# Kernel tuning notes

Hardware: AMD Instinct MI355X
Metric: run time of the kernel (lower is better)

Reference implementation:

```python
import jax, jax.numpy as jnp
import numpy as np

B, S, D, H = 4, 2048, 1024, 16
DH = D // H
SCALE = float(np.sqrt(DH))


def setup_inputs() -> dict:
    key = jax.random.key(0)
    ks = jax.random.split(key, 5)
    std = 1.0 / np.sqrt(D)
    return {
        "x": jax.random.normal(ks[0], (B, S, D), dtype=jnp.float32),
        "Wq": jax.random.normal(ks[1], (D, D), dtype=jnp.float32) * std,
        "bq": jnp.zeros((D,), dtype=jnp.float32),
        "Wk": jax.random.normal(ks[2], (D, D), dtype=jnp.float32) * std,
        "bk": jnp.zeros((D,), dtype=jnp.float32),
        "Wv": jax.random.normal(ks[3], (D, D), dtype=jnp.float32) * std,
        "bv": jnp.zeros((D,), dtype=jnp.float32),
        "Wo": jax.random.normal(ks[4], (D, D), dtype=jnp.float32) * std,
        "bo": jnp.zeros((D,), dtype=jnp.float32),
        "padding_mask": jnp.ones((B, S), dtype=jnp.int32),
    }


def reference(x, Wq, bq, Wk, bk, Wv, bv, Wo, bo, padding_mask):
    b, s, d = x.shape
    # QKV projections, split heads -> [b, h, s, dh]
    q = (x @ Wq + bq).reshape(b, s, H, DH).transpose(0, 2, 1, 3)
    k = (x @ Wk + bk).reshape(b, s, H, DH).transpose(0, 2, 1, 3)
    v = (x @ Wv + bv).reshape(b, s, H, DH).transpose(0, 2, 1, 3)
    # scaled scores [b, h, s, s]
    scores = jnp.einsum('bhqd,bhkd->bhqk', q, k) / SCALE
    neg_inf = jnp.float32(-jnp.inf)
    causal = jnp.tril(jnp.ones((s, s), dtype=bool))  # [s, s]
    scores = jnp.where(causal[None, None, :, :], scores, neg_inf)
    pad = (padding_mask != 0)[:, None, None, :]  # [b,1,1,s] on key axis
    scores = jnp.where(pad, scores, neg_inf)
    weights = jax.nn.softmax(scores, axis=-1)
    weights = jnp.nan_to_num(weights, nan=0.0)  # fully-masked rows -> 0
    # dropout is identity in eval / p=0
    attended = jnp.einsum('bhqk,bhkd->bhqd', weights, v)
    attended = attended.transpose(0, 2, 1, 3).reshape(b, s, d)
    return attended @ Wo + bo
```

## Files before the change

kernel.cpp:

```cpp
#include <hip/hip_runtime.h>
#include <hip/hip_bf16.h>

#define B_   4
#define S_   2048
#define D_   1024
#define H_   16
#define DH_  64
#define M_   (B_ * S_)

typedef __attribute__((ext_vector_type(8))) short  bfrag8;
typedef __attribute__((ext_vector_type(4))) float  facc4;
typedef unsigned short u16;
typedef unsigned long long u64;

__device__ __forceinline__ u16 f2bf(float f) {
    union { __hip_bfloat16 h; u16 u; } c;
    c.h = __float2bfloat16(f);
    return c.u;
}

__device__ __forceinline__ u16 bfr(float f) {
    unsigned b = __float_as_uint(f);
    return (u16)((b + 0x7FFFu + ((b >> 16) & 1u)) >> 16);
}

__device__ __forceinline__ void gl_lds16(const u16* g, u16* l) {
    __builtin_amdgcn_global_load_lds((const __attribute__((address_space(1))) void*)g,
                                     (__attribute__((address_space(3))) void*)l,
                                     16, 0, 0);
}

__global__ __launch_bounds__(256) void prep(const float* __restrict__ x, u16* __restrict__ X16,
                                            const float* __restrict__ w0, const float* __restrict__ w1,
                                            const float* __restrict__ w2, const float* __restrict__ w3,
                                            u16* __restrict__ o0, u16* __restrict__ o1,
                                            u16* __restrict__ o2, u16* __restrict__ o3) {
    __shared__ u16 t[32][33];
    int bid = blockIdx.x;
    if (bid < 4096) {
        int i = (bid * 256 + threadIdx.x) * 8;
        float4 v0 = *(const float4*)(x + i);
        float4 v1 = *(const float4*)(x + i + 4);
        ushort4 r0, r1;
        r0.x = f2bf(v0.x); r0.y = f2bf(v0.y); r0.z = f2bf(v0.z); r0.w = f2bf(v0.w);
        r1.x = f2bf(v1.x); r1.y = f2bf(v1.y); r1.z = f2bf(v1.z); r1.w = f2bf(v1.w);
        *(ushort4*)(X16 + i) = r0;
        *(ushort4*)(X16 + i + 4) = r1;
    } else {
        int lid = bid - 4096;
        int z = lid >> 10, r = lid & 1023;
        const float* w; u16* o;
        switch (z) {
            case 0: w = w0; o = o0; break;
            case 1: w = w1; o = o1; break;
            case 2: w = w2; o = o2; break;
            default: w = w3; o = o3; break;
        }
        int kb = (r >> 5) * 32, nb = (r & 31) * 32;
        int c = threadIdx.x & 31, r0 = threadIdx.x >> 5;
#pragma unroll
        for (int i = 0; i < 4; i++) {
            int rr = r0 + 8 * i;
            t[rr][c] = f2bf(w[(kb + rr) * D_ + nb + c]);
        }
        __syncthreads();
#pragma unroll
        for (int i = 0; i < 4; i++) {
            int rr = r0 + 8 * i;
            o[(nb + rr) * D_ + kb + c] = t[c][rr];
        }
    }
}

#define ABUF_ (256 * 32)
#define TBUF_ ((256 + 128) * 32)
#define NKT_  32

__device__ __forceinline__ void gemm_body256(const u16* __restrict__ A,
                                             const u16* __restrict__ BT,
                                             const float* __restrict__ bias,
                                             void* __restrict__ Cout, int mode, float scale,
                                             u16* S, int nb, int mb) {
    int tid = threadIdx.x;
    int w = tid >> 6, lane = tid & 63, quad = lane >> 4, l16 = lane & 15;
    int wm = (w >> 1) * 64, wn = (w & 1) * 64;
    int x3 = l16 & 3;

    const u16* Aga[2]; const u16* Bga;
#pragma unroll
    for (int i = 0; i < 2; ++i) {
        int idx = i * 512 + tid, row = idx >> 2;
        int lu = (idx & 3) ^ (row & 3);
        Aga[i] = A + (size_t)(mb + row) * D_ + lu * 8;
    }
    {
        int row = tid >> 2;
        int lu = (tid & 3) ^ (row & 3);
        Bga = BT + (size_t)(nb + row) * D_ + lu * 8;
    }

    facc4 acc[4][4] = {};

    u16* Bu0 = S;
    u16* Bu1 = S + TBUF_;
    u16* Bu2 = S + 2 * TBUF_;

    auto stage = [&](u16* Nb, int ko) {
#pragma unroll
        for (int i = 0; i < 2; ++i) gl_lds16(Aga[i] + ko, Nb + (i * 512 + tid) * 8);
        gl_lds16(Bga + ko, Nb + ABUF_ + tid * 8);
    };
    auto compute = [&](const u16* Cb) {
        int pu = (quad ^ x3) * 8;
        bfrag8 af[4], bf[4];
#pragma unroll
        for (int mt = 0; mt < 4; ++mt)
            af[mt] = *(const bfrag8*)(Cb + (wm + mt * 16 + l16) * 32 + pu);
#pragma unroll
        for (int nt = 0; nt < 4; ++nt)
            bf[nt] = *(const bfrag8*)(Cb + ABUF_ + (wn + nt * 16 + l16) * 32 + pu);
        __builtin_amdgcn_s_setprio(1);
#pragma unroll
        for (int mt = 0; mt < 4; ++mt)
#pragma unroll
            for (int nt = 0; nt < 4; ++nt)
                acc[mt][nt] = __builtin_amdgcn_mfma_f32_16x16x32_bf16(af[mt], bf[nt], acc[mt][nt], 0, 0, 0);
        __builtin_amdgcn_s_setprio(0);
    };

    stage(Bu0, 0);
    stage(Bu1, 32);

    u16 *bc = Bu0, *bn = Bu1, *bs = Bu2;
    for (int kt = 0; kt < NKT_; ++kt) {
        if (kt < NKT_ - 1) asm volatile("s_waitcnt vmcnt(3)" ::: "memory");
        else               asm volatile("s_waitcnt vmcnt(0)" ::: "memory");
        __builtin_amdgcn_sched_barrier(0);
        __builtin_amdgcn_s_barrier();
        __builtin_amdgcn_sched_barrier(0);
        if (kt + 2 < NKT_) stage(bs, (kt + 2) * 32);
        compute(bc);
        u16* tmp = bc; bc = bn; bn = bs; bs = tmp;
    }

#pragma unroll
    for (int mt = 0; mt < 4; ++mt) {
        int m_base = mb + wm + mt * 16 + quad * 4;
#pragma unroll
        for (int nt = 0; nt < 4; ++nt) {
            int n = nb + wn + nt * 16 + l16;
            float bv = bias[n];
            int h = n >> 6, dd = n & 63;
#pragma unroll
            for (int r = 0; r < 4; ++r) {
                int m = m_base + r;
                float v = (acc[mt][nt][r] + bv) * scale;
                int bi = m >> 11, s = m & (S_ - 1);
                if (mode == 0) {
                    ((u16*)Cout)[(((bi * H_ + h) * S_) + s) * DH_ + dd] = bfr(v);
                } else if (mode == 1) {
                    ((u16*)Cout)[(((bi * H_ + h) * DH_) + dd) * S_ + s] = bfr(v);
                } else {
                    ((float*)Cout)[(size_t)m * D_ + n] = v;
                }
            }
        }
    }
}

#define CE_Q 0.18033688011112042f

__global__ __launch_bounds__(512, 4) void gemm_qkv(const u16* __restrict__ A,
                                                const u16* __restrict__ WTq, const float* __restrict__ bq, u16* __restrict__ Qb,
                                                const u16* __restrict__ WTk, const float* __restrict__ bk, u16* __restrict__ Kb,
                                                const u16* __restrict__ WTv, const float* __restrict__ bv, u16* __restrict__ VTb) {
    __shared__ __attribute__((aligned(16))) u16 Sh[3 * TBUF_];
    int lid = blockIdx.x;
    int xcd = lid & 7, s = lid >> 3;
    int z = s >> 5, inner = s & 31;
    int mb = (xcd * 4 + (inner >> 3)) * 256;
    int nb = (inner & 7) * 128;
    switch (z) {
        case 0: gemm_body256(A, WTq, bq, Qb, 0, CE_Q, Sh, nb, mb); break;
        case 1: gemm_body256(A, WTk, bk, Kb, 0, 1.0f, Sh, nb, mb); break;
        default: gemm_body256(A, WTv, bv, VTb, 1, 1.0f, Sh, nb, mb); break;
    }
}

__global__ __launch_bounds__(512, 4) void gemm_o(const u16* __restrict__ A,
                                              const u16* __restrict__ WTo, const float* __restrict__ bo,
                                              float* __restrict__ out) {
    __shared__ __attribute__((aligned(16))) u16 Sh[3 * TBUF_];
    int lid = blockIdx.x;
    int xcd = lid & 7, s = lid >> 3;
    int mb = (xcd * 4 + (s >> 3)) * 256;
    int nb = (s & 7) * 128;
    gemm_body256(A, WTo, bo, out, 2, 1.0f, Sh, nb, mb);
}

__device__ __forceinline__ void soft_pv(const float* p, float& lp, facc4* oaccq,
                                        const bfrag8* vf, int a0, int a1, bool qlo) {
    float rs = 0.f;
    unsigned pk[4];
#pragma unroll
    for (int j = 0; j < 4; ++j) {
        float e0 = exp2f(p[2 * j]);
        float e1 = exp2f(p[2 * j + 1]);
        rs += e0; rs += e1;
        pk[j] = __builtin_amdgcn_perm(__float_as_uint(e1), __float_as_uint(e0), 0x07060302u);
    }
    lp += rs;
    union { unsigned d[4]; bfrag8 v; } pb;
    {
        unsigned lo, hi;
        lo = __builtin_amdgcn_ds_bpermute(a0, (int)pk[0]);
        hi = __builtin_amdgcn_ds_bpermute(a0, (int)pk[2]);
        pb.d[0] = qlo ? lo : hi;
        lo = __builtin_amdgcn_ds_bpermute(a0, (int)pk[1]);
        hi = __builtin_amdgcn_ds_bpermute(a0, (int)pk[3]);
        pb.d[1] = qlo ? lo : hi;
        lo = __builtin_amdgcn_ds_bpermute(a1, (int)pk[0]);
        hi = __builtin_amdgcn_ds_bpermute(a1, (int)pk[2]);
        pb.d[2] = qlo ? lo : hi;
        lo = __builtin_amdgcn_ds_bpermute(a1, (int)pk[1]);
        hi = __builtin_amdgcn_ds_bpermute(a1, (int)pk[3]);
        pb.d[3] = qlo ? lo : hi;
    }
    __builtin_amdgcn_s_setprio(1);
#pragma unroll
    for (int dt = 0; dt < 4; ++dt)
        oaccq[dt] = __builtin_amdgcn_mfma_f32_16x16x32_bf16(vf[dt], pb.v, oaccq[dt], 0, 0, 0);
    __builtin_amdgcn_s_setprio(0);
}

__global__ __launch_bounds__(256, 4) void attn(const u16* __restrict__ Q,
                                               const u16* __restrict__ K,
                                               const u16* __restrict__ VT,
                                               const int* __restrict__ pm,
                                               u16* __restrict__ Aout) {
    __shared__ __attribute__((aligned(16))) u16 Ks[2][32 * 64];
    __shared__ __attribute__((aligned(16))) u16 Vs[2][64 * 32];
    __shared__ unsigned pms[64];

    int tid = threadIdx.x, w = tid >> 6, lane = tid & 63;
    int quad = lane >> 4, l16 = lane & 15;

    int lid = blockIdx.x;
    int bh  = (lid & 7) * 8 + ((lid >> 3) & 7);
    int g   = lid >> 6;
    int gq = g >> 2, gr = g & 3;
    int ci = (gq == 0) ? 15 - gr : (gq == 1) ? gr : (gq == 2) ? 11 - gr : 4 + gr;
    int b = bh >> 4, h = bh & 15;

    int qbase = ci * 128;
    int qw = qbase + w * 32;
    int tmax = (qbase >> 5) + 3;

    const u16* Qp = Q + (size_t)(b * H_ + h) * S_ * DH_;
    const u16* Kp = K + (size_t)(b * H_ + h) * S_ * DH_;
    const u16* Vp = VT + (size_t)(b * H_ + h) * DH_ * S_;
    u16* Ao = Aout + (size_t)b * S_ * D_ + h * DH_;

#pragma unroll
    for (int i = 0; i < 8; ++i) {
        int j2 = w * 16 + i * 2;
        u64 m = __ballot(pm[b * S_ + j2 * 32 + lane] != 0);
        if (lane == 0) { pms[j2] = (unsigned)m; pms[j2 + 1] = (unsigned)(m >> 32); }
    }

    int krow = tid >> 3, ku = tid & 7;
    const u16* Kg = Kp + krow * DH_ + ((ku ^ (krow & 7)) * 8);
    int vrow = tid >> 2, vu = tid & 3;
    const u16* Vg = Vp + vrow * S_ + ((vu ^ (vrow & 3)) * 8);
    u16* Kl[2] = { &Ks[0][tid * 8], &Ks[1][tid * 8] };
    u16* Vl[2] = { &Vs[0][tid * 8], &Vs[1][tid * 8] };

    int k7 = l16 & 7, v3 = l16 & 3;

    int a0 = ((((2 * quad) & 3) * 16 + l16) << 2);
    int a1 = ((((2 * quad + 1) & 3) * 16 + l16) << 2);
    bool qlo = quad < 2;

    bfrag8 qf[2][2];
#pragma unroll
    for (int qt = 0; qt < 2; ++qt)
#pragma unroll
        for (int cc = 0; cc < 2; ++cc)
            qf[qt][cc] = *(const bfrag8*)(Qp + (qw + qt * 16 + l16) * DH_ + cc * 32 + quad * 8);

    facc4 oacc[2][4] = {};
    float lp[2] = {0.f, 0.f};

    gl_lds16(Kg, Kl[0]);
    gl_lds16(Vg, Vl[0]);
    __syncthreads();
    unsigned vmn = pms[0];

    for (int t = 0; t <= tmax; ++t) {
        int cur = t & 1, nxt = cur ^ 1;
        unsigned vm = vmn;
        if (t < tmax) {
            int k1 = (t + 1) * 32;
            gl_lds16(Kg + k1 * DH_, Kl[nxt]);
            gl_lds16(Vg + k1, Vl[nxt]);
            vmn = pms[t + 1];
        }
        int k0 = t * 32;
        const u16* Kc = Ks[cur];
        const u16* Vc = Vs[cur];

        bfrag8 kf00 = *(const bfrag8*)(Kc + (l16 * 8        + ((quad)     ^ k7)) * 8);
        bfrag8 kf01 = *(const bfrag8*)(Kc + (l16 * 8        + ((quad + 4) ^ k7)) * 8);
        bfrag8 kf10 = *(const bfrag8*)(Kc + ((l16 + 16) * 8 + ((quad)     ^ k7)) * 8);
        bfrag8 kf11 = *(const bfrag8*)(Kc + ((l16 + 16) * 8 + ((quad + 4) ^ k7)) * 8);
        bfrag8 vf[4];
#pragma unroll
        for (int dt = 0; dt < 4; ++dt)
            vf[dt] = *(const bfrag8*)(Vc + ((dt * 16 + l16) * 4 + (quad ^ v3)) * 8);

        facc4 st[2][2] = {};
        __builtin_amdgcn_s_setprio(1);
#pragma unroll
        for (int qt = 0; qt < 2; ++qt) {
            st[qt][0] = __builtin_amdgcn_mfma_f32_16x16x32_bf16(kf00, qf[qt][0], st[qt][0], 0, 0, 0);
            st[qt][0] = __builtin_amdgcn_mfma_f32_16x16x32_bf16(kf01, qf[qt][1], st[qt][0], 0, 0, 0);
            st[qt][1] = __builtin_amdgcn_mfma_f32_16x16x32_bf16(kf10, qf[qt][0], st[qt][1], 0, 0, 0);
            st[qt][1] = __builtin_amdgcn_mfma_f32_16x16x32_bf16(kf11, qf[qt][1], st[qt][1], 0, 0, 0);
        }
        __builtin_amdgcn_s_setprio(0);

        if (vm == 0xffffffffu && k0 + 31 < qw) {
#pragma unroll
            for (int qt = 0; qt < 2; ++qt) {
                float p[8];
#pragma unroll
                for (int kt = 0; kt < 2; ++kt)
#pragma unroll
                    for (int r = 0; r < 4; ++r) p[kt * 4 + r] = st[qt][kt][r];
                soft_pv(p, lp[qt], oacc[qt], vf, a0, a1, qlo);
            }
        } else {
#pragma unroll
            for (int qt = 0; qt < 2; ++qt) {
                int q0 = qw + qt * 16;
                float p[8];
#pragma unroll
                for (int kt = 0; kt < 2; ++kt)
#pragma unroll
                    for (int r = 0; r < 4; ++r) {
                        int kl = kt * 16 + quad * 4 + r;
                        bool ok = ((vm >> kl) & 1u) && (k0 + kl <= q0 + l16);
                        p[kt * 4 + r] = ok ? st[qt][kt][r] : -1e30f;
                    }
                soft_pv(p, lp[qt], oacc[qt], vf, a0, a1, qlo);
            }
        }
        __syncthreads();
    }

#pragma unroll
    for (int qt = 0; qt < 2; ++qt) {
        float l = lp[qt];
        l += __shfl_xor(l, 16);
        l += __shfl_xor(l, 32);
        float linv = (l > 0.f) ? 1.f / l : 0.f;
        size_t qoff = (size_t)(qw + qt * 16 + l16) * D_;
#pragma unroll
        for (int dt = 0; dt < 4; ++dt) {
            union { u16 hh[4]; u64 q; } pk4;
#pragma unroll
            for (int r = 0; r < 4; ++r) pk4.hh[r] = bfr(oacc[qt][dt][r] * linv);
            *(u64*)(Ao + qoff + dt * 16 + quad * 4) = pk4.q;
        }
    }
}

extern "C" void kernel_launch(void* const* d_in, const int* in_sizes, int n_in,
                              void* d_out, int out_size, void* d_ws, size_t ws_size,
                              hipStream_t stream) {
    const float* x  = (const float*)d_in[0];
    const float* Wq = (const float*)d_in[1];
    const float* bq = (const float*)d_in[2];
    const float* Wk = (const float*)d_in[3];
    const float* bk = (const float*)d_in[4];
    const float* Wv = (const float*)d_in[5];
    const float* bv = (const float*)d_in[6];
    const float* Wo = (const float*)d_in[7];
    const float* bo = (const float*)d_in[8];
    const int*   pm = (const int*)d_in[9];
    float* out = (float*)d_out;

    char* ws = (char*)d_ws;
    const size_t SZ_XD = (size_t)M_ * D_ * 2;
    const size_t SZ_W  = (size_t)D_ * D_ * 2;
    u16* X16 = (u16*)ws;
    u16* WTq = (u16*)(ws + SZ_XD);
    u16* WTk = (u16*)(ws + SZ_XD + SZ_W);
    u16* WTv = (u16*)(ws + SZ_XD + 2 * SZ_W);
    u16* WTo = (u16*)(ws + SZ_XD + 3 * SZ_W);
    u16* Qb  = (u16*)(ws + SZ_XD + 4 * SZ_W);
    u16* Kb  = (u16*)(ws + 2 * SZ_XD + 4 * SZ_W);
    u16* VTb = (u16*)(ws + 3 * SZ_XD + 4 * SZ_W);
    u16* Att = X16;

    prep<<<dim3(8192), 256, 0, stream>>>(x, X16, Wq, Wk, Wv, Wo, WTq, WTk, WTv, WTo);

    gemm_qkv<<<dim3(768), 512, 0, stream>>>(X16, WTq, bq, Qb, WTk, bk, Kb, WTv, bv, VTb);

    attn<<<dim3(1024), 256, 0, stream>>>(Qb, Kb, VTb, pm, Att);

    gemm_o<<<dim3(256), 512, 0, stream>>>(Att, WTo, bo, out);
}
```

Before: 254.7 us.

## Shrink GEMM tiles to 128x128 and stage two K/V tiles per attention iteration

The projection GEMMs move from 256x128 tiles with 512 threads to 128x128 tiles with 256 threads, doubling the grid so the output GEMM gets 512 blocks instead of 256 and fills the CUs better. The attention kernel now loads 64 keys per pipeline stage (two 32-key sub-tiles) and processes both before each barrier, halving the number of syncthreads and global-to-LDS round trips. The cost is less operand reuse per GEMM tile, more LDS per attention block, and a coarser causal loop bound that may process some extra masked keys.

```diff
diff --git a/kernel.cpp b/kernel.cpp
--- a/kernel.cpp
+++ b/kernel.cpp
@@ -72,11 +72,11 @@
     }
 }
 
-#define ABUF_ (256 * 32)
-#define TBUF_ ((256 + 128) * 32)
-#define NKT_  32
-
-__device__ __forceinline__ void gemm_body256(const u16* __restrict__ A,
+#define AB2_ (128 * 32)
+#define TB2_ (256 * 32)
+#define NKT_ 32
+
+__device__ __forceinline__ void gemm_body128(const u16* __restrict__ A,
                                              const u16* __restrict__ BT,
                                              const float* __restrict__ bias,
                                              void* __restrict__ Cout, int mode, float scale,
@@ -86,29 +86,26 @@
     int wm = (w >> 1) * 64, wn = (w & 1) * 64;
     int x3 = l16 & 3;
 
-    const u16* Aga[2]; const u16* Bga;
+    const u16* Aga[2]; const u16* Bga[2];
 #pragma unroll
     for (int i = 0; i < 2; ++i) {
-        int idx = i * 512 + tid, row = idx >> 2;
+        int idx = i * 256 + tid, row = idx >> 2;
         int lu = (idx & 3) ^ (row & 3);
         Aga[i] = A + (size_t)(mb + row) * D_ + lu * 8;
-    }
-    {
-        int row = tid >> 2;
-        int lu = (tid & 3) ^ (row & 3);
-        Bga = BT + (size_t)(nb + row) * D_ + lu * 8;
+        Bga[i] = BT + (size_t)(nb + row) * D_ + lu * 8;
     }
 
     facc4 acc[4][4] = {};
 
     u16* Bu0 = S;
-    u16* Bu1 = S + TBUF_;
-    u16* Bu2 = S + 2 * TBUF_;
+    u16* Bu1 = S + TB2_;
+    u16* Bu2 = S + 2 * TB2_;
 
     auto stage = [&](u16* Nb, int ko) {
 #pragma unroll
-        for (int i = 0; i < 2; ++i) gl_lds16(Aga[i] + ko, Nb + (i * 512 + tid) * 8);
-        gl_lds16(Bga + ko, Nb + ABUF_ + tid * 8);
+        for (int i = 0; i < 2; ++i) gl_lds16(Aga[i] + ko, Nb + (i * 256 + tid) * 8);
+#pragma unroll
+        for (int i = 0; i < 2; ++i) gl_lds16(Bga[i] + ko, Nb + AB2_ + (i * 256 + tid) * 8);
     };
     auto compute = [&](const u16* Cb) {
         int pu = (quad ^ x3) * 8;
@@ -118,7 +115,7 @@
             af[mt] = *(const bfrag8*)(Cb + (wm + mt * 16 + l16) * 32 + pu);
 #pragma unroll
         for (int nt = 0; nt < 4; ++nt)
-            bf[nt] = *(const bfrag8*)(Cb + ABUF_ + (wn + nt * 16 + l16) * 32 + pu);
+            bf[nt] = *(const bfrag8*)(Cb + AB2_ + (wn + nt * 16 + l16) * 32 + pu);
         __builtin_amdgcn_s_setprio(1);
 #pragma unroll
         for (int mt = 0; mt < 4; ++mt)
@@ -133,7 +130,7 @@
 
     u16 *bc = Bu0, *bn = Bu1, *bs = Bu2;
     for (int kt = 0; kt < NKT_; ++kt) {
-        if (kt < NKT_ - 1) asm volatile("s_waitcnt vmcnt(3)" ::: "memory");
+        if (kt < NKT_ - 1) asm volatile("s_waitcnt vmcnt(4)" ::: "memory");
         else               asm volatile("s_waitcnt vmcnt(0)" ::: "memory");
         __builtin_amdgcn_sched_barrier(0);
         __builtin_amdgcn_s_barrier();
@@ -170,32 +167,32 @@
 
 #define CE_Q 0.18033688011112042f
 
-__global__ __launch_bounds__(512, 4) void gemm_qkv(const u16* __restrict__ A,
+__global__ __launch_bounds__(256, 3) void gemm_qkv(const u16* __restrict__ A,
                                                 const u16* __restrict__ WTq, const float* __restrict__ bq, u16* __restrict__ Qb,
                                                 const u16* __restrict__ WTk, const float* __restrict__ bk, u16* __restrict__ Kb,
                                                 const u16* __restrict__ WTv, const float* __restrict__ bv, u16* __restrict__ VTb) {
-    __shared__ __attribute__((aligned(16))) u16 Sh[3 * TBUF_];
+    __shared__ __attribute__((aligned(16))) u16 Sh[3 * TB2_];
     int lid = blockIdx.x;
-    int xcd = lid & 7, s = lid >> 3;
-    int z = s >> 5, inner = s & 31;
-    int mb = (xcd * 4 + (inner >> 3)) * 256;
-    int nb = (inner & 7) * 128;
+    int xcd = lid & 7, rest = lid >> 3;
+    int z = rest >> 6, r2 = rest & 63;
+    int mb = (xcd * 8 + (r2 >> 3)) * 128;
+    int nb = (r2 & 7) * 128;
     switch (z) {
-        case 0: gemm_body256(A, WTq, bq, Qb, 0, CE_Q, Sh, nb, mb); break;
-        case 1: gemm_body256(A, WTk, bk, Kb, 0, 1.0f, Sh, nb, mb); break;
-        default: gemm_body256(A, WTv, bv, VTb, 1, 1.0f, Sh, nb, mb); break;
-    }
-}
-
-__global__ __launch_bounds__(512, 4) void gemm_o(const u16* __restrict__ A,
+        case 0: gemm_body128(A, WTq, bq, Qb, 0, CE_Q, Sh, nb, mb); break;
+        case 1: gemm_body128(A, WTk, bk, Kb, 0, 1.0f, Sh, nb, mb); break;
+        default: gemm_body128(A, WTv, bv, VTb, 1, 1.0f, Sh, nb, mb); break;
+    }
+}
+
+__global__ __launch_bounds__(256, 3) void gemm_o(const u16* __restrict__ A,
                                               const u16* __restrict__ WTo, const float* __restrict__ bo,
                                               float* __restrict__ out) {
-    __shared__ __attribute__((aligned(16))) u16 Sh[3 * TBUF_];
+    __shared__ __attribute__((aligned(16))) u16 Sh[3 * TB2_];
     int lid = blockIdx.x;
-    int xcd = lid & 7, s = lid >> 3;
-    int mb = (xcd * 4 + (s >> 3)) * 256;
-    int nb = (s & 7) * 128;
-    gemm_body256(A, WTo, bo, out, 2, 1.0f, Sh, nb, mb);
+    int xcd = lid & 7, r2 = lid >> 3;
+    int mb = (xcd * 8 + (r2 >> 3)) * 128;
+    int nb = (r2 & 7) * 128;
+    gemm_body128(A, WTo, bo, out, 2, 1.0f, Sh, nb, mb);
 }
 
 __device__ __forceinline__ void soft_pv(const float* p, float& lp, facc4* oaccq,
@@ -238,8 +235,8 @@
                                                const u16* __restrict__ VT,
                                                const int* __restrict__ pm,
                                                u16* __restrict__ Aout) {
-    __shared__ __attribute__((aligned(16))) u16 Ks[2][32 * 64];
-    __shared__ __attribute__((aligned(16))) u16 Vs[2][64 * 32];
+    __shared__ __attribute__((aligned(16))) u16 Ks[2][2][32 * 64];
+    __shared__ __attribute__((aligned(16))) u16 Vs[2][2][64 * 32];
     __shared__ unsigned pms[64];
 
     int tid = threadIdx.x, w = tid >> 6, lane = tid & 63;
@@ -254,7 +251,7 @@
 
     int qbase = ci * 128;
     int qw = qbase + w * 32;
-    int tmax = (qbase >> 5) + 3;
+    int tmax = (qbase >> 6) + 1;
 
     const u16* Qp = Q + (size_t)(b * H_ + h) * S_ * DH_;
     const u16* Kp = K + (size_t)(b * H_ + h) * S_ * DH_;
@@ -272,8 +269,6 @@
     const u16* Kg = Kp + krow * DH_ + ((ku ^ (krow & 7)) * 8);
     int vrow = tid >> 2, vu = tid & 3;
     const u16* Vg = Vp + vrow * S_ + ((vu ^ (vrow & 3)) * 8);
-    u16* Kl[2] = { &Ks[0][tid * 8], &Ks[1][tid * 8] };
-    u16* Vl[2] = { &Vs[0][tid * 8], &Vs[1][tid * 8] };
 
     int k7 = l16 & 7, v3 = l16 & 3;
 
@@ -291,68 +286,74 @@
     facc4 oacc[2][4] = {};
     float lp[2] = {0.f, 0.f};
 
-    gl_lds16(Kg, Kl[0]);
-    gl_lds16(Vg, Vl[0]);
+    gl_lds16(Kg, &Ks[0][0][tid * 8]);
+    gl_lds16(Kg + 32 * DH_, &Ks[0][1][tid * 8]);
+    gl_lds16(Vg, &Vs[0][0][tid * 8]);
+    gl_lds16(Vg + 32, &Vs[0][1][tid * 8]);
     __syncthreads();
-    unsigned vmn = pms[0];
 
     for (int t = 0; t <= tmax; ++t) {
         int cur = t & 1, nxt = cur ^ 1;
-        unsigned vm = vmn;
         if (t < tmax) {
-            int k1 = (t + 1) * 32;
-            gl_lds16(Kg + k1 * DH_, Kl[nxt]);
-            gl_lds16(Vg + k1, Vl[nxt]);
-            vmn = pms[t + 1];
-        }
-        int k0 = t * 32;
-        const u16* Kc = Ks[cur];
-        const u16* Vc = Vs[cur];
-
-        bfrag8 kf00 = *(const bfrag8*)(Kc + (l16 * 8        + ((quad)     ^ k7)) * 8);
-        bfrag8 kf01 = *(const bfrag8*)(Kc + (l16 * 8        + ((quad + 4) ^ k7)) * 8);
-        bfrag8 kf10 = *(const bfrag8*)(Kc + ((l16 + 16) * 8 + ((quad)     ^ k7)) * 8);
-        bfrag8 kf11 = *(const bfrag8*)(Kc + ((l16 + 16) * 8 + ((quad + 4) ^ k7)) * 8);
-        bfrag8 vf[4];
-#pragma unroll
-        for (int dt = 0; dt < 4; ++dt)
-            vf[dt] = *(const bfrag8*)(Vc + ((dt * 16 + l16) * 4 + (quad ^ v3)) * 8);
-
-        facc4 st[2][2] = {};
-        __builtin_amdgcn_s_setprio(1);
-#pragma unroll
-        for (int qt = 0; qt < 2; ++qt) {
-            st[qt][0] = __builtin_amdgcn_mfma_f32_16x16x32_bf16(kf00, qf[qt][0], st[qt][0], 0, 0, 0);
-            st[qt][0] = __builtin_amdgcn_mfma_f32_16x16x32_bf16(kf01, qf[qt][1], st[qt][0], 0, 0, 0);
-            st[qt][1] = __builtin_amdgcn_mfma_f32_16x16x32_bf16(kf10, qf[qt][0], st[qt][1], 0, 0, 0);
-            st[qt][1] = __builtin_amdgcn_mfma_f32_16x16x32_bf16(kf11, qf[qt][1], st[qt][1], 0, 0, 0);
-        }
-        __builtin_amdgcn_s_setprio(0);
-
-        if (vm == 0xffffffffu && k0 + 31 < qw) {
+            int k1 = (t + 1) * 64;
+            gl_lds16(Kg + k1 * DH_, &Ks[nxt][0][tid * 8]);
+            gl_lds16(Kg + (k1 + 32) * DH_, &Ks[nxt][1][tid * 8]);
+            gl_lds16(Vg + k1, &Vs[nxt][0][tid * 8]);
+            gl_lds16(Vg + k1 + 32, &Vs[nxt][1][tid * 8]);
+        }
+
+#pragma unroll
+        for (int s = 0; s < 2; ++s) {
+            int k0 = t * 64 + s * 32;
+            const u16* Kc = Ks[cur][s];
+            const u16* Vc = Vs[cur][s];
+            unsigned vm = pms[2 * t + s];
+
+            bfrag8 kf00 = *(const bfrag8*)(Kc + (l16 * 8        + ((quad)     ^ k7)) * 8);
+            bfrag8 kf01 = *(const bfrag8*)(Kc + (l16 * 8        + ((quad + 4) ^ k7)) * 8);
+            bfrag8 kf10 = *(const bfrag8*)(Kc + ((l16 + 16) * 8 + ((quad)     ^ k7)) * 8);
+            bfrag8 kf11 = *(const bfrag8*)(Kc + ((l16 + 16) * 8 + ((quad + 4) ^ k7)) * 8);
+            bfrag8 vf[4];
+#pragma unroll
+            for (int dt = 0; dt < 4; ++dt)
+                vf[dt] = *(const bfrag8*)(Vc + ((dt * 16 + l16) * 4 + (quad ^ v3)) * 8);
+
+            facc4 st[2][2] = {};
+            __builtin_amdgcn_s_setprio(1);
 #pragma unroll
             for (int qt = 0; qt < 2; ++qt) {
-                float p[8];
-#pragma unroll
-                for (int kt = 0; kt < 2; ++kt)
-#pragma unroll
-                    for (int r = 0; r < 4; ++r) p[kt * 4 + r] = st[qt][kt][r];
-                soft_pv(p, lp[qt], oacc[qt], vf, a0, a1, qlo);
+                st[qt][0] = __builtin_amdgcn_mfma_f32_16x16x32_bf16(kf00, qf[qt][0], st[qt][0], 0, 0, 0);
+                st[qt][0] = __builtin_amdgcn_mfma_f32_16x16x32_bf16(kf01, qf[qt][1], st[qt][0], 0, 0, 0);
+                st[qt][1] = __builtin_amdgcn_mfma_f32_16x16x32_bf16(kf10, qf[qt][0], st[qt][1], 0, 0, 0);
+                st[qt][1] = __builtin_amdgcn_mfma_f32_16x16x32_bf16(kf11, qf[qt][1], st[qt][1], 0, 0, 0);
             }
-        } else {
-#pragma unroll
-            for (int qt = 0; qt < 2; ++qt) {
-                int q0 = qw + qt * 16;
-                float p[8];
-#pragma unroll
-                for (int kt = 0; kt < 2; ++kt)
-#pragma unroll
-                    for (int r = 0; r < 4; ++r) {
-                        int kl = kt * 16 + quad * 4 + r;
-                        bool ok = ((vm >> kl) & 1u) && (k0 + kl <= q0 + l16);
-                        p[kt * 4 + r] = ok ? st[qt][kt][r] : -1e30f;
-                    }
-                soft_pv(p, lp[qt], oacc[qt], vf, a0, a1, qlo);
+            __builtin_amdgcn_s_setprio(0);
+
+            if (vm == 0xffffffffu && k0 + 31 < qw) {
+#pragma unroll
+                for (int qt = 0; qt < 2; ++qt) {
+                    float p[8];
+#pragma unroll
+                    for (int kt = 0; kt < 2; ++kt)
+#pragma unroll
+                        for (int r = 0; r < 4; ++r) p[kt * 4 + r] = st[qt][kt][r];
+                    soft_pv(p, lp[qt], oacc[qt], vf, a0, a1, qlo);
+                }
+            } else {
+#pragma unroll
+                for (int qt = 0; qt < 2; ++qt) {
+                    int q0 = qw + qt * 16;
+                    float p[8];
+#pragma unroll
+                    for (int kt = 0; kt < 2; ++kt)
+#pragma unroll
+                        for (int r = 0; r < 4; ++r) {
+                            int kl = kt * 16 + quad * 4 + r;
+                            bool ok = ((vm >> kl) & 1u) && (k0 + kl <= q0 + l16);
+                            p[kt * 4 + r] = ok ? st[qt][kt][r] : -1e30f;
+                        }
+                    soft_pv(p, lp[qt], oacc[qt], vf, a0, a1, qlo);
+                }
             }
         }
         __syncthreads();
@@ -405,9 +406,9 @@
 
     prep<<<dim3(8192), 256, 0, stream>>>(x, X16, Wq, Wk, Wv, Wo, WTq, WTk, WTv, WTo);
 
-    gemm_qkv<<<dim3(768), 512, 0, stream>>>(X16, WTq, bq, Qb, WTk, bk, Kb, WTv, bv, VTb);
+    gemm_qkv<<<dim3(1536), 256, 0, stream>>>(X16, WTq, bq, Qb, WTk, bk, Kb, WTv, bv, VTb);
 
     attn<<<dim3(1024), 256, 0, stream>>>(Qb, Kb, VTb, pm, Att);
 
-    gemm_o<<<dim3(256), 512, 0, stream>>>(Att, WTo, bo, out);
-}
+    gemm_o<<<dim3(512), 256, 0, stream>>>(Att, WTo, bo, out);
+}
```

After: 293.2 us. +15.1%, slower.
